# Performance work log

Measured on AMD Instinct MI355X. Metric: run time of the kernel, lower is better.

Reference implementation:

```python
import jax, jax.numpy as jnp
import numpy as np

MARGIN_SCALE = 0.2
SPATIAL_ALPHA = 0.6
CHANNEL_ALPHA = 0.5
LANG_ALPHA = 0.4
EPS = 1e-06


def _xywh_to_xyxy(boxes):
    xc, yc, w, h = jnp.split(boxes, 4, axis=-1)
    return jnp.concatenate([xc - w / 2.0, yc - h / 2.0, xc + w / 2.0, yc + h / 2.0], axis=-1)


def _clamp_boxes(boxes):
    x1, y1, x2, y2 = [jnp.clip(b[..., 0], 0.0, 1.0) for b in jnp.split(boxes, 4, axis=-1)]
    x_low, x_high = jnp.minimum(x1, x2), jnp.maximum(x1, x2)
    y_low, y_high = jnp.minimum(y1, y2), jnp.maximum(y1, y2)
    w = jnp.maximum(x_high - x_low, EPS)
    h = jnp.maximum(y_high - y_low, EPS)
    cx = (x_high + x_low) * 0.5
    cy = (y_high + y_low) * 0.5
    return jnp.stack([
        jnp.clip(cx - w * 0.5, 0.0, 1.0),
        jnp.clip(cy - h * 0.5, 0.0, 1.0),
        jnp.clip(cx + w * 0.5, 0.0, 1.0),
        jnp.clip(cy + h * 0.5, 0.0, 1.0),
    ], axis=-1)


def _box_to_mask(boxes_xyxy, H, W, margin, dtype):
    # fully vectorized replacement of the per-sample Python loop
    ys = jnp.linspace(0.0, 1.0, H)  # [H]
    xs = jnp.linspace(0.0, 1.0, W)  # [W]
    x1, y1, x2, y2 = [boxes_xyxy[:, i] for i in range(4)]
    mx1 = jnp.clip(x1 - margin, 0.0, 1.0)[:, None, None]
    my1 = jnp.clip(y1 - margin, 0.0, 1.0)[:, None, None]
    mx2 = jnp.clip(x2 + margin, 0.0, 1.0)[:, None, None]
    my2 = jnp.clip(y2 + margin, 0.0, 1.0)[:, None, None]
    xg = xs[None, None, :]  # [1,1,W]
    yg = ys[None, :, None]  # [1,H,1]
    mask = (xg >= mx1) & (xg <= mx2) & (yg >= my1) & (yg <= my2)  # [B,H,W]
    return mask.astype(dtype)[:, None, :, :]  # [B,1,H,W]


def _conv2d(x, w, b, pad):
    out = jax.lax.conv_general_dilated(
        x, w, window_strides=(1, 1), padding=((pad, pad), (pad, pad)),
        dimension_numbers=('NCHW', 'OIHW', 'NCHW'))
    return out + b[None, :, None, None]


def setup_inputs() -> dict:
    key = jax.random.key(0)
    ks = jax.random.split(key, 9)
    B, C, H, W = 32, 256, 64, 64
    s = lambda fan_in: 1.0 / np.sqrt(fan_in)
    return {
        'feat': jax.random.normal(ks[0], (B, C, H, W), jnp.float32),
        'lang_vec': jax.random.normal(ks[1], (B, 256), jnp.float32),
        'pointer_xywh': jax.random.uniform(ks[2], (B, 4), jnp.float32),
        'conv1_w': jax.random.normal(ks[3], (16, 1, 3, 3), jnp.float32) * s(9),
        'conv1_b': jnp.zeros((16,), jnp.float32),
        'conv2_w': jax.random.normal(ks[4], (1, 16, 1, 1), jnp.float32) * s(16),
        'conv2_b': jnp.zeros((1,), jnp.float32),
        'cg_w1': jax.random.normal(ks[5], (256, 512), jnp.float32) * s(512),
        'cg_b1': jnp.zeros((256,), jnp.float32),
        'cg_w2': jax.random.normal(ks[6], (256, 256), jnp.float32) * s(256),
        'cg_b2': jnp.zeros((256,), jnp.float32),
        'lf_w1': jax.random.normal(ks[7], (256, 512), jnp.float32) * s(512),
        'lf_b1': jnp.zeros((256,), jnp.float32),
        'lf_w2': jax.random.normal(ks[8], (256, 256), jnp.float32) * s(256),
        'lf_b2': jnp.zeros((256,), jnp.float32),
    }


def reference(feat, lang_vec, pointer_xywh, conv1_w, conv1_b, conv2_w, conv2_b,
              cg_w1, cg_b1, cg_w2, cg_b2, lf_w1, lf_b1, lf_w2, lf_b2):
    B, C, H, W = feat.shape
    boxes_xyxy = _clamp_boxes(_xywh_to_xyxy(pointer_xywh))
    w = jnp.maximum(boxes_xyxy[:, 2] - boxes_xyxy[:, 0], 1e-4)
    h = jnp.maximum(boxes_xyxy[:, 3] - boxes_xyxy[:, 1], 1e-4)
    diag = jnp.sqrt(w * w + h * h)
    margin = jnp.clip(diag * MARGIN_SCALE, 0.02, 0.2)
    mask = _box_to_mask(boxes_xyxy, H, W, margin, feat.dtype)  # [B,1,H,W]

    # spatial gate: conv3x3 -> relu -> conv1x1 -> sigmoid
    hidden = jax.nn.relu(_conv2d(mask, conv1_w, conv1_b, pad=1))
    refined_mask = jax.nn.sigmoid(_conv2d(hidden, conv2_w, conv2_b, pad=0))  # [B,1,H,W]

    mask_area = jnp.maximum(refined_mask.sum(axis=(2, 3)), 1.0)  # [B,1]
    pointer_feat = (feat * refined_mask).sum(axis=(2, 3)) / mask_area  # [B,C]

    fusion = jnp.concatenate([pointer_feat, lang_vec], axis=1)  # [B, C+256]
    ch_gate = jax.nn.sigmoid(jax.nn.relu(fusion @ cg_w1.T + cg_b1) @ cg_w2.T + cg_b2)
    ch_gate = ch_gate.reshape(B, C, 1, 1)
    lang_delta = jnp.tanh(jax.nn.relu(fusion @ lf_w1.T + lf_b1) @ lf_w2.T + lf_b2)

    guided_feat = feat * (1.0 + SPATIAL_ALPHA * refined_mask) * (1.0 + CHANNEL_ALPHA * ch_gate)
    guided_lang = lang_vec + LANG_ALPHA * lang_delta
    return (guided_feat, guided_lang, boxes_xyxy, refined_mask, pointer_feat)
```

## Files before the change

kernel.cpp:

```cpp
#include <hip/hip_runtime.h>
#include <math.h>

#define B_  32
#define C_  256
#define H_  64
#define W_  64
#define HW  (H_*W_)
#define HW4 (HW/4)
#define RPB 4

typedef float f32x4 __attribute__((ext_vector_type(4)));

__device__ __forceinline__ float clamp01(float v) {
    return fminf(fmaxf(v, 0.0f), 1.0f);
}

__global__ __launch_bounds__(256) void kern_mask(
    const float* __restrict__ xywh,
    const float* __restrict__ conv1_w, const float* __restrict__ conv1_b,
    const float* __restrict__ conv2_w, const float* __restrict__ conv2_b,
    float* __restrict__ out_boxes, float* __restrict__ out_rm,
    float* __restrict__ ws_part)
{
    const int b = blockIdx.x >> 2;
    const int q = blockIdx.x & 3;
    const int t = threadIdx.x;

    __shared__ float sw1[16 * 9];
    __shared__ float sb1[16];
    __shared__ float sw2[16];
    __shared__ float sred[4];

    if (t < 144)                 sw1[t]       = conv1_w[t];
    else if (t < 160)            sb1[t - 144] = conv1_b[t - 144];
    else if (t < 176)            sw2[t - 160] = conv2_w[t - 160];
    const float b2v = conv2_b[0];

    const float xc = xywh[b * 4 + 0];
    const float yc = xywh[b * 4 + 1];
    const float bw = xywh[b * 4 + 2];
    const float bh = xywh[b * 4 + 3];

    float x1 = clamp01(xc - bw * 0.5f);
    float y1 = clamp01(yc - bh * 0.5f);
    float x2 = clamp01(xc + bw * 0.5f);
    float y2 = clamp01(yc + bh * 0.5f);
    float xl = fminf(x1, x2), xh = fmaxf(x1, x2);
    float yl = fminf(y1, y2), yh = fmaxf(y1, y2);
    float w_ = fmaxf(xh - xl, 1e-6f);
    float h_ = fmaxf(yh - yl, 1e-6f);
    float cx = (xh + xl) * 0.5f, cy = (yh + yl) * 0.5f;
    float bx1 = clamp01(cx - w_ * 0.5f);
    float by1 = clamp01(cy - h_ * 0.5f);
    float bx2 = clamp01(cx + w_ * 0.5f);
    float by2 = clamp01(cy + h_ * 0.5f);

    if (t == 0 && q == 0) {
        out_boxes[b * 4 + 0] = bx1;
        out_boxes[b * 4 + 1] = by1;
        out_boxes[b * 4 + 2] = bx2;
        out_boxes[b * 4 + 3] = by2;
    }

    float ww = fmaxf(bx2 - bx1, 1e-4f);
    float hh = fmaxf(by2 - by1, 1e-4f);
    float diag = sqrtf(ww * ww + hh * hh);
    float margin = fminf(fmaxf(diag * 0.2f, 0.02f), 0.2f);
    float mx1 = clamp01(bx1 - margin);
    float my1 = clamp01(by1 - margin);
    float mx2 = clamp01(bx2 + margin);
    float my2 = clamp01(by2 + margin);

    __syncthreads();

    float asum = 0.0f;
    const int p0 = q * 1024;
    for (int pi = t; pi < 1024; pi += 256) {
        const int p = p0 + pi;
        const int y = p >> 6;
        const int x = p & 63;
        float mv[9];
        #pragma unroll
        for (int ky = 0; ky < 3; ++ky) {
            const int yy = y + ky - 1;
            float gy = (float)((double)yy / 63.0);
            bool yin = (yy >= 0) && (yy < H_) && (gy >= my1) && (gy <= my2);
            #pragma unroll
            for (int kx = 0; kx < 3; ++kx) {
                const int xx = x + kx - 1;
                float gx = (float)((double)xx / 63.0);
                bool xin = (xx >= 0) && (xx < W_) && (gx >= mx1) && (gx <= mx2);
                mv[ky * 3 + kx] = (yin && xin) ? 1.0f : 0.0f;
            }
        }
        float z = b2v;
        #pragma unroll
        for (int oc = 0; oc < 16; ++oc) {
            float hsum = sb1[oc];
            #pragma unroll
            for (int k = 0; k < 9; ++k) hsum = fmaf(mv[k], sw1[oc * 9 + k], hsum);
            z = fmaf(fmaxf(hsum, 0.0f), sw2[oc], z);
        }
        float rm = 1.0f / (1.0f + expf(-z));
        out_rm[b * HW + p] = rm;
        asum += rm;
    }

    #pragma unroll
    for (int off = 32; off > 0; off >>= 1) asum += __shfl_down(asum, off, 64);
    int lane = t & 63, wid = t >> 6;
    if (lane == 0) sred[wid] = asum;
    __syncthreads();
    if (t == 0) ws_part[b * 4 + q] = sred[0] + sred[1] + sred[2] + sred[3];
}

__global__ __launch_bounds__(256) void kern_pf(
    const float* __restrict__ feat, const float* __restrict__ rm,
    const float* __restrict__ ws_part, float* __restrict__ out_pf)
{
    const int blk = blockIdx.x;
    const int b = blk >> 6;
    const int c0 = (blk & 63) * RPB;
    __shared__ f32x4 sred[4];

    const size_t row0 = ((size_t)b * C_ + c0) * HW;
    const f32x4* fr = (const f32x4*)(feat + row0);
    const f32x4* r4 = (const f32x4*)(rm + (size_t)b * HW);

    float s0 = 0.f, s1 = 0.f, s2 = 0.f, s3 = 0.f;
    for (int i = threadIdx.x; i < HW4; i += 256) {
        f32x4 r = r4[i];
        f32x4 f0 = fr[i];
        f32x4 f1 = fr[i + HW4];
        f32x4 f2 = fr[i + 2 * HW4];
        f32x4 f3 = fr[i + 3 * HW4];
        s0 = fmaf(f0.x, r.x, fmaf(f0.y, r.y, fmaf(f0.z, r.z, fmaf(f0.w, r.w, s0))));
        s1 = fmaf(f1.x, r.x, fmaf(f1.y, r.y, fmaf(f1.z, r.z, fmaf(f1.w, r.w, s1))));
        s2 = fmaf(f2.x, r.x, fmaf(f2.y, r.y, fmaf(f2.z, r.z, fmaf(f2.w, r.w, s2))));
        s3 = fmaf(f3.x, r.x, fmaf(f3.y, r.y, fmaf(f3.z, r.z, fmaf(f3.w, r.w, s3))));
    }

    #pragma unroll
    for (int off = 32; off > 0; off >>= 1) {
        s0 += __shfl_down(s0, off, 64);
        s1 += __shfl_down(s1, off, 64);
        s2 += __shfl_down(s2, off, 64);
        s3 += __shfl_down(s3, off, 64);
    }
    int lane = threadIdx.x & 63, wid = threadIdx.x >> 6;
    if (lane == 0) { f32x4 v; v.x = s0; v.y = s1; v.z = s2; v.w = s3; sred[wid] = v; }
    __syncthreads();
    if (threadIdx.x == 0) {
        float area = fmaxf(ws_part[b * 4 + 0] + ws_part[b * 4 + 1] +
                           ws_part[b * 4 + 2] + ws_part[b * 4 + 3], 1.0f);
        float inv = 1.0f / area;
        f32x4 t0 = sred[0], t1 = sred[1], t2 = sred[2], t3 = sred[3];
        out_pf[b * C_ + c0 + 0] = (t0.x + t1.x + t2.x + t3.x) * inv;
        out_pf[b * C_ + c0 + 1] = (t0.y + t1.y + t2.y + t3.y) * inv;
        out_pf[b * C_ + c0 + 2] = (t0.z + t1.z + t2.z + t3.z) * inv;
        out_pf[b * C_ + c0 + 3] = (t0.w + t1.w + t2.w + t3.w) * inv;
    }
}

__global__ __launch_bounds__(256) void kern_mlp(
    const float* __restrict__ pf, const float* __restrict__ lang,
    const float* __restrict__ cg_w1, const float* __restrict__ cg_b1,
    const float* __restrict__ cg_w2, const float* __restrict__ cg_b2,
    const float* __restrict__ lf_w1, const float* __restrict__ lf_b1,
    const float* __restrict__ lf_w2, const float* __restrict__ lf_b2,
    float* __restrict__ ws_cg, float* __restrict__ out_gl)
{
    const int b = blockIdx.x >> 1;
    const int which = blockIdx.x & 1;
    const int t = threadIdx.x;
    __shared__ float fus[512];
    __shared__ float hid[256];

    fus[t]       = pf[b * 256 + t];
    fus[256 + t] = lang[b * 256 + t];

    const float* w1 = which ? lf_w1 : cg_w1;
    const float* b1 = which ? lf_b1 : cg_b1;
    const float* w2 = which ? lf_w2 : cg_w2;
    const float* b2 = which ? lf_b2 : cg_b2;
    __syncthreads();

    const f32x4* wv = (const f32x4*)(w1 + (size_t)t * 512);
    const f32x4* fv = (const f32x4*)fus;
    float s = 0.0f;
    #pragma unroll 4
    for (int k = 0; k < 128; ++k) {
        f32x4 f = fv[k], w = wv[k];
        s = fmaf(f.x, w.x, fmaf(f.y, w.y, fmaf(f.z, w.z, fmaf(f.w, w.w, s))));
    }
    hid[t] = fmaxf(s + b1[t], 0.0f);
    __syncthreads();

    const f32x4* w2v = (const f32x4*)(w2 + (size_t)t * 256);
    const f32x4* hv = (const f32x4*)hid;
    float s2 = 0.0f;
    #pragma unroll 4
    for (int k = 0; k < 64; ++k) {
        f32x4 h = hv[k], w = w2v[k];
        s2 = fmaf(h.x, w.x, fmaf(h.y, w.y, fmaf(h.z, w.z, fmaf(h.w, w.w, s2))));
    }
    s2 += b2[t];
    if (which == 0) {
        ws_cg[b * 256 + t] = 1.0f + 0.5f / (1.0f + expf(-s2));
    } else {
        out_gl[b * 256 + t] = fus[256 + t] + 0.4f * tanhf(s2);
    }
}

__global__ __launch_bounds__(256) void kern_guided(
    const float* __restrict__ feat, const float* __restrict__ rm,
    const float* __restrict__ ws_cg, float* __restrict__ out_gf)
{
    const int blk = blockIdx.x;
    const int b = blk >> 6;
    const int c0 = (blk & 63) * RPB;
    const float g0 = ws_cg[b * C_ + c0 + 0];
    const float g1 = ws_cg[b * C_ + c0 + 1];
    const float g2 = ws_cg[b * C_ + c0 + 2];
    const float g3 = ws_cg[b * C_ + c0 + 3];

    const size_t row0 = ((size_t)b * C_ + c0) * HW;
    const f32x4* fr = (const f32x4*)(feat + row0);
    f32x4* orow = (f32x4*)(out_gf + row0);
    const f32x4* r4 = (const f32x4*)(rm + (size_t)b * HW);

    for (int i = threadIdx.x; i < HW4; i += 256) {
        f32x4 r = r4[i];
        f32x4 m;
        m.x = 1.0f + 0.6f * r.x;
        m.y = 1.0f + 0.6f * r.y;
        m.z = 1.0f + 0.6f * r.z;
        m.w = 1.0f + 0.6f * r.w;
        f32x4 f0 = fr[i];
        f32x4 f1 = fr[i + HW4];
        f32x4 f2 = fr[i + 2 * HW4];
        f32x4 f3 = fr[i + 3 * HW4];
        f32x4 o0, o1, o2, o3;
        o0.x = f0.x * m.x * g0; o0.y = f0.y * m.y * g0;
        o0.z = f0.z * m.z * g0; o0.w = f0.w * m.w * g0;
        o1.x = f1.x * m.x * g1; o1.y = f1.y * m.y * g1;
        o1.z = f1.z * m.z * g1; o1.w = f1.w * m.w * g1;
        o2.x = f2.x * m.x * g2; o2.y = f2.y * m.y * g2;
        o2.z = f2.z * m.z * g2; o2.w = f2.w * m.w * g2;
        o3.x = f3.x * m.x * g3; o3.y = f3.y * m.y * g3;
        o3.z = f3.z * m.z * g3; o3.w = f3.w * m.w * g3;
        __builtin_nontemporal_store(o0, &orow[i]);
        __builtin_nontemporal_store(o1, &orow[i + HW4]);
        __builtin_nontemporal_store(o2, &orow[i + 2 * HW4]);
        __builtin_nontemporal_store(o3, &orow[i + 3 * HW4]);
    }
}

extern "C" void kernel_launch(void* const* d_in, const int* in_sizes, int n_in,
                              void* d_out, int out_size, void* d_ws, size_t ws_size,
                              hipStream_t stream) {
    const float* feat     = (const float*)d_in[0];
    const float* lang     = (const float*)d_in[1];
    const float* xywh     = (const float*)d_in[2];
    const float* conv1_w  = (const float*)d_in[3];
    const float* conv1_b  = (const float*)d_in[4];
    const float* conv2_w  = (const float*)d_in[5];
    const float* conv2_b  = (const float*)d_in[6];
    const float* cg_w1    = (const float*)d_in[7];
    const float* cg_b1    = (const float*)d_in[8];
    const float* cg_w2    = (const float*)d_in[9];
    const float* cg_b2    = (const float*)d_in[10];
    const float* lf_w1    = (const float*)d_in[11];
    const float* lf_b1    = (const float*)d_in[12];
    const float* lf_w2    = (const float*)d_in[13];
    const float* lf_b2    = (const float*)d_in[14];

    float* out = (float*)d_out;
    const size_t N_GF = (size_t)B_ * C_ * HW;
    float* out_gf    = out;
    float* out_gl    = out_gf + N_GF;
    float* out_boxes = out_gl + (size_t)B_ * C_;
    float* out_rm    = out_boxes + B_ * 4;
    float* out_pf    = out_rm + (size_t)B_ * HW;

    float* wsf     = (float*)d_ws;
    float* ws_part = wsf;
    float* ws_cg   = wsf + 128;

    (void)ws_size; (void)in_sizes; (void)n_in; (void)out_size;

    kern_mask<<<B_ * 4, 256, 0, stream>>>(xywh, conv1_w, conv1_b, conv2_w, conv2_b,
                                          out_boxes, out_rm, ws_part);
    kern_pf<<<B_ * C_ / RPB, 256, 0, stream>>>(feat, out_rm, ws_part, out_pf);
    kern_mlp<<<B_ * 2, 256, 0, stream>>>(out_pf, lang,
                                         cg_w1, cg_b1, cg_w2, cg_b2,
                                         lf_w1, lf_b1, lf_w2, lf_b2,
                                         ws_cg, out_gl);
    kern_guided<<<B_ * C_ / RPB, 256, 0, stream>>>(feat, out_rm, ws_cg, out_gf);
}
```

Measured before the change: 95.00 us.

## Fuse mask computation into pointer-feature kernel using separable pattern lookup table

Drops the separate mask kernel. Each pointer-feature block now recomputes the refined mask in LDS, using a 64-entry lookup table indexed by the 3-bit x and y neighbourhood patterns, so the 16-channel convolution runs only 64 times per block instead of once per pixel. This removes one launch and the global round trip of the mask before the reduction. The cost is redundant mask recomputation across the 64 blocks per batch and 16KB of LDS per block, which may lower occupancy. Also adds unroll-2 hints on the streaming loops.

```diff
diff --git a/kernel.cpp b/kernel.cpp
--- a/kernel.cpp
+++ b/kernel.cpp
@@ -15,21 +15,30 @@
     return fminf(fmaxf(v, 0.0f), 1.0f);
 }
 
-__global__ __launch_bounds__(256) void kern_mask(
-    const float* __restrict__ xywh,
+__global__ __launch_bounds__(256) void kern_pf(
+    const float* __restrict__ feat, const float* __restrict__ xywh,
     const float* __restrict__ conv1_w, const float* __restrict__ conv1_b,
     const float* __restrict__ conv2_w, const float* __restrict__ conv2_b,
     float* __restrict__ out_boxes, float* __restrict__ out_rm,
-    float* __restrict__ ws_part)
+    float* __restrict__ out_pf)
 {
-    const int b = blockIdx.x >> 2;
-    const int q = blockIdx.x & 3;
+    const int blk = blockIdx.x;
+    const int b = blk >> 6;
+    const int g = blk & 63;
+    const int c0 = g * RPB;
     const int t = threadIdx.x;
 
     __shared__ float sw1[16 * 9];
     __shared__ float sb1[16];
     __shared__ float sw2[16];
-    __shared__ float sred[4];
+    __shared__ float tbl[64];
+    __shared__ int   xpat[64];
+    __shared__ int   ypat[64];
+    __shared__ f32x4 rm4_lds[HW4];
+    __shared__ float sreda[4];
+    __shared__ f32x4 sredv[4];
+
+    float* rm_lds = (float*)rm4_lds;
 
     if (t < 144)                 sw1[t]       = conv1_w[t];
     else if (t < 160)            sb1[t - 144] = conv1_b[t - 144];
@@ -55,7 +64,7 @@
     float bx2 = clamp01(cx + w_ * 0.5f);
     float by2 = clamp01(cy + h_ * 0.5f);
 
-    if (t == 0 && q == 0) {
+    if (t == 0 && g == 0) {
         out_boxes[b * 4 + 0] = bx1;
         out_boxes[b * 4 + 1] = by1;
         out_boxes[b * 4 + 2] = bx2;
@@ -73,26 +82,37 @@
 
     __syncthreads();
 
-    float asum = 0.0f;
-    const int p0 = q * 1024;
-    for (int pi = t; pi < 1024; pi += 256) {
-        const int p = p0 + pi;
-        const int y = p >> 6;
-        const int x = p & 63;
+    if (t < 64) {
+        const int x = t;
+        int p = 0;
+        #pragma unroll
+        for (int k = 0; k < 3; ++k) {
+            const int xx = x + k - 1;
+            float gx = (float)((double)xx / 63.0);
+            bool in = (xx >= 0) && (xx < W_) && (gx >= mx1) && (gx <= mx2);
+            p |= (in ? 1 : 0) << k;
+        }
+        xpat[x] = p;
+    } else if (t < 128) {
+        const int y = t - 64;
+        int p = 0;
+        #pragma unroll
+        for (int k = 0; k < 3; ++k) {
+            const int yy = y + k - 1;
+            float gy = (float)((double)yy / 63.0);
+            bool in = (yy >= 0) && (yy < H_) && (gy >= my1) && (gy <= my2);
+            p |= (in ? 1 : 0) << k;
+        }
+        ypat[y] = p;
+    } else if (t < 192) {
+        const int e = t - 128;
+        const int xp = e & 7, yp = e >> 3;
         float mv[9];
         #pragma unroll
-        for (int ky = 0; ky < 3; ++ky) {
-            const int yy = y + ky - 1;
-            float gy = (float)((double)yy / 63.0);
-            bool yin = (yy >= 0) && (yy < H_) && (gy >= my1) && (gy <= my2);
+        for (int ky = 0; ky < 3; ++ky)
             #pragma unroll
-            for (int kx = 0; kx < 3; ++kx) {
-                const int xx = x + kx - 1;
-                float gx = (float)((double)xx / 63.0);
-                bool xin = (xx >= 0) && (xx < W_) && (gx >= mx1) && (gx <= mx2);
-                mv[ky * 3 + kx] = (yin && xin) ? 1.0f : 0.0f;
-            }
-        }
+            for (int kx = 0; kx < 3; ++kx)
+                mv[ky * 3 + kx] = (((yp >> ky) & 1) && ((xp >> kx) & 1)) ? 1.0f : 0.0f;
         float z = b2v;
         #pragma unroll
         for (int oc = 0; oc < 16; ++oc) {
@@ -101,35 +121,35 @@
             for (int k = 0; k < 9; ++k) hsum = fmaf(mv[k], sw1[oc * 9 + k], hsum);
             z = fmaf(fmaxf(hsum, 0.0f), sw2[oc], z);
         }
-        float rm = 1.0f / (1.0f + expf(-z));
-        out_rm[b * HW + p] = rm;
+        tbl[e] = 1.0f / (1.0f + expf(-z));
+    }
+    __syncthreads();
+
+    float asum = 0.0f;
+    for (int p = t; p < HW; p += 256) {
+        const int y = p >> 6;
+        const int x = p & 63;
+        float rm = tbl[ypat[y] * 8 + xpat[x]];
+        rm_lds[p] = rm;
         asum += rm;
     }
-
     #pragma unroll
     for (int off = 32; off > 0; off >>= 1) asum += __shfl_down(asum, off, 64);
-    int lane = t & 63, wid = t >> 6;
-    if (lane == 0) sred[wid] = asum;
-    __syncthreads();
-    if (t == 0) ws_part[b * 4 + q] = sred[0] + sred[1] + sred[2] + sred[3];
-}
-
-__global__ __launch_bounds__(256) void kern_pf(
-    const float* __restrict__ feat, const float* __restrict__ rm,
-    const float* __restrict__ ws_part, float* __restrict__ out_pf)
-{
-    const int blk = blockIdx.x;
-    const int b = blk >> 6;
-    const int c0 = (blk & 63) * RPB;
-    __shared__ f32x4 sred[4];
-
-    const size_t row0 = ((size_t)b * C_ + c0) * HW;
-    const f32x4* fr = (const f32x4*)(feat + row0);
-    const f32x4* r4 = (const f32x4*)(rm + (size_t)b * HW);
-
+    const int lane = t & 63, wid = t >> 6;
+    if (lane == 0) sreda[wid] = asum;
+    __syncthreads();
+    const float inv = 1.0f / fmaxf(sreda[0] + sreda[1] + sreda[2] + sreda[3], 1.0f);
+
+    if (g == 0) {
+        f32x4* orm = (f32x4*)(out_rm + (size_t)b * HW);
+        for (int i = t; i < HW4; i += 256) orm[i] = rm4_lds[i];
+    }
+
+    const f32x4* fr = (const f32x4*)(feat + ((size_t)b * C_ + c0) * HW);
     float s0 = 0.f, s1 = 0.f, s2 = 0.f, s3 = 0.f;
-    for (int i = threadIdx.x; i < HW4; i += 256) {
-        f32x4 r = r4[i];
+    #pragma unroll 2
+    for (int i = t; i < HW4; i += 256) {
+        f32x4 r = rm4_lds[i];
         f32x4 f0 = fr[i];
         f32x4 f1 = fr[i + HW4];
         f32x4 f2 = fr[i + 2 * HW4];
@@ -147,14 +167,10 @@
         s2 += __shfl_down(s2, off, 64);
         s3 += __shfl_down(s3, off, 64);
     }
-    int lane = threadIdx.x & 63, wid = threadIdx.x >> 6;
-    if (lane == 0) { f32x4 v; v.x = s0; v.y = s1; v.z = s2; v.w = s3; sred[wid] = v; }
-    __syncthreads();
-    if (threadIdx.x == 0) {
-        float area = fmaxf(ws_part[b * 4 + 0] + ws_part[b * 4 + 1] +
-                           ws_part[b * 4 + 2] + ws_part[b * 4 + 3], 1.0f);
-        float inv = 1.0f / area;
-        f32x4 t0 = sred[0], t1 = sred[1], t2 = sred[2], t3 = sred[3];
+    if (lane == 0) { f32x4 v; v.x = s0; v.y = s1; v.z = s2; v.w = s3; sredv[wid] = v; }
+    __syncthreads();
+    if (t == 0) {
+        f32x4 t0 = sredv[0], t1 = sredv[1], t2 = sredv[2], t3 = sredv[3];
         out_pf[b * C_ + c0 + 0] = (t0.x + t1.x + t2.x + t3.x) * inv;
         out_pf[b * C_ + c0 + 1] = (t0.y + t1.y + t2.y + t3.y) * inv;
         out_pf[b * C_ + c0 + 2] = (t0.z + t1.z + t2.z + t3.z) * inv;
@@ -229,6 +245,7 @@
     f32x4* orow = (f32x4*)(out_gf + row0);
     const f32x4* r4 = (const f32x4*)(rm + (size_t)b * HW);
 
+    #pragma unroll 2
     for (int i = threadIdx.x; i < HW4; i += 256) {
         f32x4 r = r4[i];
         f32x4 m;
@@ -283,15 +300,14 @@
     float* out_rm    = out_boxes + B_ * 4;
     float* out_pf    = out_rm + (size_t)B_ * HW;
 
-    float* wsf     = (float*)d_ws;
-    float* ws_part = wsf;
-    float* ws_cg   = wsf + 128;
+    float* wsf   = (float*)d_ws;
+    float* ws_cg = wsf;
 
     (void)ws_size; (void)in_sizes; (void)n_in; (void)out_size;
 
-    kern_mask<<<B_ * 4, 256, 0, stream>>>(xywh, conv1_w, conv1_b, conv2_w, conv2_b,
-                                          out_boxes, out_rm, ws_part);
-    kern_pf<<<B_ * C_ / RPB, 256, 0, stream>>>(feat, out_rm, ws_part, out_pf);
+    kern_pf<<<B_ * C_ / RPB, 256, 0, stream>>>(feat, xywh,
+                                               conv1_w, conv1_b, conv2_w, conv2_b,
+                                               out_boxes, out_rm, out_pf);
     kern_mlp<<<B_ * 2, 256, 0, stream>>>(out_pf, lang,
                                          cg_w1, cg_b1, cg_w2, cg_b2,
                                          lf_w1, lf_b1, lf_w2, lf_b2,
```

After: 95.09 us. About the same (+0.1%).
